# Optimization experiments

Hardware: AMD Instinct MI355X
Metric: run time of the kernel (lower is better)

The kernel has to match this reference:

```python
import jax, jax.numpy as jnp
import numpy as np

B, L, DIM, HEAD_DIM, COND = 16, 1025, 1024, 64, 256
N_HEADS = DIM // HEAD_DIM
EPS = 1e-6


def _make_cos_sin():
    # freqs: head_dim//8 log-spaced frequencies in [pi, 10*pi]
    freqs = np.exp(np.linspace(np.log(np.pi), np.log(10 * np.pi), HEAD_DIM // 8)).astype(np.float32)
    # axial positions on a 32x32 grid (cell centers in [-1, 1]), with a zero pos prepended
    g = np.linspace(-1.0, 1.0, 33, dtype=np.float32)
    g = (g[:-1] + g[1:]) / 2
    hh, ww = np.meshgrid(g, g, indexing='ij')
    pos = np.stack([hh.ravel(), ww.ravel()], axis=-1)          # [1024, 2]
    pos = np.concatenate([np.zeros((1, 2), np.float32), pos])  # [1025, 2]
    theta = np.concatenate([pos[:, 0:1] * freqs, pos[:, 1:2] * freqs], axis=-1)  # [L, head_dim//4]
    return jnp.asarray(np.cos(theta)), jnp.asarray(np.sin(theta))


def setup_inputs() -> dict:
    key = jax.random.key(0)
    kx, kc, kn, kq, ko = jax.random.split(key, 5)
    cos, sin = _make_cos_sin()
    return {
        'x': jax.random.normal(kx, (B, L, DIM), jnp.float32),
        'cond': jax.random.normal(kc, (B, COND), jnp.float32),
        'w_norm': jax.random.normal(kn, (DIM, COND), jnp.float32) * 0.02,   # AdaRMSNorm linear (zero-init in training; random here)
        'w_qkv': jax.random.normal(kq, (3 * DIM, DIM), jnp.float32) * 0.02,
        'w_out': jax.random.normal(ko, (DIM, DIM), jnp.float32) * 0.02,
        'cos': cos,  # [L, head_dim//4]
        'sin': sin,
    }


def _rope(t, cos, sin):
    # partial non-interleaved rotary: rotate first 2*cos.shape[-1] dims, leave the rest
    half = cos.shape[-1]                      # head_dim//4
    t1 = t[..., :half]
    t2 = t[..., half:2 * half]
    rest = t[..., 2 * half:]
    c = cos[None, :, None, :]                 # [1, L, 1, half]
    s = sin[None, :, None, :]
    return jnp.concatenate([t1 * c - t2 * s, t2 * c + t1 * s, rest], axis=-1)


def reference(x, cond, w_norm, w_qkv, w_out, cos, sin):
    skip = x
    # AdaRMSNorm: scale = cond-linear + 1, normalized by rms(x) in fp32
    scale = cond @ w_norm.T + 1.0                                    # [B, D]
    mean_sq = jnp.mean(jnp.square(x.astype(jnp.float32)), axis=-1, keepdims=True)
    xn = x * (scale[:, None, :] * jax.lax.rsqrt(mean_sq + EPS)).astype(x.dtype)
    # QKV projection
    qkv = (xn @ w_qkv.T).reshape(B, L, 3, N_HEADS, HEAD_DIM)
    q, k, v = qkv[:, :, 0], qkv[:, :, 1], qkv[:, :, 2]               # [B, L, H, hd]
    q = _rope(q, cos, sin)
    k = _rope(k, cos, sin)
    # causal attention (flash_attn default softmax scale = head_dim**-0.5)
    sm_scale = 1.0 / jnp.sqrt(jnp.asarray(HEAD_DIM, jnp.float32))
    scores = jnp.einsum('blhd,bmhd->bhlm', q, k) * sm_scale
    causal = jnp.tril(jnp.ones((L, L), bool))
    scores = jnp.where(causal[None, None], scores, jnp.finfo(scores.dtype).min)
    attn = jax.nn.softmax(scores, axis=-1)
    o = jnp.einsum('bhlm,bmhd->blhd', attn, v).reshape(B, L, DIM)
    return o @ w_out.T + skip
```

## Files before the change

kernel.cpp:

```cpp
#include <hip/hip_runtime.h>
#include <hip/hip_bf16.h>
#include <cstdint>

typedef __bf16 bf16;
typedef bf16 bf16x4 __attribute__((ext_vector_type(4)));
typedef bf16 bf16x8 __attribute__((ext_vector_type(8)));
typedef float f32x4 __attribute__((ext_vector_type(4)));
typedef float f32x16 __attribute__((ext_vector_type(16)));
typedef uint32_t u32x4 __attribute__((ext_vector_type(4)));

#define NB 16
#define NL 1025
#define NDIM 1024
#define NHEADS 16
#define NCOND 256
#define NBH (NB*NHEADS)
#define NML (NB*NL)
#define LP 1056
#define NSLOT 17
#define QSCALE (0.125f * 1.44269504088896340736f)

__device__ __forceinline__ void gload16(const void* g, void* l) {
  __builtin_amdgcn_global_load_lds(
      (const __attribute__((address_space(1))) void*)(uintptr_t)g,
      (__attribute__((address_space(3))) void*)(uintptr_t)l,
      16, 0, 0);
}

__device__ __forceinline__ float fexp2(float x) {
  return __builtin_amdgcn_exp2f(x);
}

__device__ __forceinline__ uint32_t cvtpk(float lo, float hi) {
  uint32_t r;
  asm("v_cvt_pk_bf16_f32 %0, %1, %2" : "=v"(r) : "v"(lo), "v"(hi));
  return r;
}

__device__ __forceinline__ f32x16 zero16() {
  f32x16 z;
#pragma unroll
  for (int i = 0; i < 16; ++i) z[i] = 0.f;
  return z;
}

__global__ __launch_bounds__(256) void k_scale(const float* __restrict__ cond,
                                               const float* __restrict__ wn,
                                               float* __restrict__ scl) {
  __shared__ float cs[NCOND];
  const int b = blockIdx.x, t = threadIdx.x;
  cs[t] = cond[b * NCOND + t];
  __syncthreads();
#pragma unroll
  for (int dd = 0; dd < 4; ++dd) {
    const int d = t * 4 + dd;
    const float4* w = (const float4*)(wn + (size_t)d * NCOND);
    float acc = 1.0f;
    for (int c4 = 0; c4 < NCOND / 4; ++c4) {
      float4 wv = w[c4];
      acc += wv.x * cs[c4*4] + wv.y * cs[c4*4+1] + wv.z * cs[c4*4+2] + wv.w * cs[c4*4+3];
    }
    scl[b * NDIM + d] = acc;
  }
}

__global__ __launch_bounds__(256) void k_cast(const float* __restrict__ src,
                                              bf16* __restrict__ dst, int n) {
  const int i = (blockIdx.x * 256 + threadIdx.x) * 4;
  if (i < n) {
    float4 v = *(const float4*)(src + i);
    bf16x4 o;
    o[0] = (bf16)v.x; o[1] = (bf16)v.y; o[2] = (bf16)v.z; o[3] = (bf16)v.w;
    *(bf16x4*)(dst + i) = o;
  }
}

__global__ __launch_bounds__(256) void k_rmsnorm(const float* __restrict__ x,
                                                 const float* __restrict__ scl,
                                                 bf16* __restrict__ xn) {
  const int row = blockIdx.x, t = threadIdx.x;
  const int b = row / NL;
  const float* xr = x + (size_t)row * NDIM;
  float4 v = *(const float4*)(xr + t * 4);
  float ss = v.x*v.x + v.y*v.y + v.z*v.z + v.w*v.w;
#pragma unroll
  for (int o = 1; o < 64; o <<= 1) ss += __shfl_xor(ss, o);
  __shared__ float red[4];
  if ((t & 63) == 0) red[t >> 6] = ss;
  __syncthreads();
  const float tot = red[0] + red[1] + red[2] + red[3];
  const float rn = rsqrtf(tot * (1.0f / NDIM) + 1e-6f);
  const float4 sc = *(const float4*)(scl + b * NDIM + t * 4);
  bf16x4 o4;
  o4[0] = (bf16)(v.x * sc.x * rn);
  o4[1] = (bf16)(v.y * sc.y * rn);
  o4[2] = (bf16)(v.z * sc.z * rn);
  o4[3] = (bf16)(v.w * sc.w * rn);
  *(bf16x4*)(xn + (size_t)row * NDIM + t * 4) = o4;
}

template <int EPI>
__global__ __launch_bounds__(256) void k_gemm(const bf16* __restrict__ A,
                                              const bf16* __restrict__ Bm,
                                              int M, int N, int K,
                                              float* __restrict__ Cf,
                                              const float* __restrict__ skip,
                                              bf16* __restrict__ qro,
                                              bf16* __restrict__ kro,
                                              bf16* __restrict__ vto,
                                              const float* __restrict__ cosT,
                                              const float* __restrict__ sinT) {
  __shared__ bf16 Als[2][128 * 64];
  __shared__ bf16 Bls[2][128 * 64];
  const int t = threadIdx.x;
  const int wave = t >> 6, lane = t & 63;
  const int g = lane >> 4, c = lane & 15;
  const int wm = wave >> 1, wn_ = wave & 1;

  const int nxb = N >> 7;
  const int nwg = gridDim.x;
  const int cpx = nwg >> 3;
  const int bid = blockIdx.x;
  const int swz = (nwg & 7) ? bid : (bid & 7) * cpx + (bid >> 3);
  const int m0 = (swz / nxb) * 128, n0 = (swz % nxb) * 128;
  const int NT = K >> 6;

  const int srow = lane >> 3;
  const int scol = ((lane & 7) ^ srow) * 8;

  f32x4 acc[4][4];
#pragma unroll
  for (int i = 0; i < 4; ++i)
#pragma unroll
    for (int j = 0; j < 4; ++j) acc[i][j] = f32x4{0.f, 0.f, 0.f, 0.f};

  auto stage = [&](int kt, int q) {
    const int k0 = kt << 6;
#pragma unroll
    for (int i = 0; i < 4; ++i) {
      const int seg = wave * 4 + i;
      int arow = m0 + seg * 8 + srow;
      if (arow >= M) arow = M - 1;
      gload16(A + (size_t)arow * K + k0 + scol, &Als[q][seg * 512]);
      const int brow = n0 + seg * 8 + srow;
      gload16(Bm + (size_t)brow * K + k0 + scol, &Bls[q][seg * 512]);
    }
  };

  stage(0, 0);
  for (int kt = 0; kt < NT; ++kt) {
    const int cur = kt & 1;
    if (kt + 1 < NT) {
      stage(kt + 1, cur ^ 1);
      asm volatile("s_waitcnt vmcnt(8)" ::: "memory");
    } else {
      asm volatile("s_waitcnt vmcnt(0)" ::: "memory");
    }
    __builtin_amdgcn_s_barrier();
    asm volatile("" ::: "memory");
#pragma unroll
    for (int kc = 0; kc < 2; ++kc) {
      bf16x8 af[4], bfr[4];
#pragma unroll
      for (int mi = 0; mi < 4; ++mi) {
        const int r = wm * 64 + mi * 16 + c;
        const int gg = ((kc * 4 + g) ^ (c & 7)) * 8;
        af[mi] = *(const bf16x8*)&Als[cur][r * 64 + gg];
      }
#pragma unroll
      for (int ni = 0; ni < 4; ++ni) {
        const int r = wn_ * 64 + ni * 16 + c;
        const int gg = ((kc * 4 + g) ^ (c & 7)) * 8;
        bfr[ni] = *(const bf16x8*)&Bls[cur][r * 64 + gg];
      }
      __builtin_amdgcn_s_setprio(1);
#pragma unroll
      for (int mi = 0; mi < 4; ++mi)
#pragma unroll
        for (int ni = 0; ni < 4; ++ni)
          acc[mi][ni] = __builtin_amdgcn_mfma_f32_16x16x32_bf16(af[mi], bfr[ni], acc[mi][ni], 0, 0, 0);
      __builtin_amdgcn_s_setprio(0);
    }
    asm volatile("" ::: "memory");
    __builtin_amdgcn_s_barrier();
  }

  if (EPI == 1) {
#pragma unroll
    for (int mi = 0; mi < 4; ++mi) {
      const int rb = m0 + wm * 64 + mi * 16 + g * 4;
#pragma unroll
      for (int ni = 0; ni < 4; ++ni) {
        const int col = n0 + wn_ * 64 + ni * 16 + c;
#pragma unroll
        for (int j = 0; j < 4; ++j) {
          const int row = rb + j;
          if (row < M) {
            const size_t idx = (size_t)row * N + col;
            Cf[idx] = acc[mi][ni][j] + skip[idx];
          }
        }
      }
    }
  } else {
    const int ncol0 = n0 + wn_ * 64;
    const int type = ncol0 >> 10;
    const int hd = (ncol0 & 1023) >> 6;
    if (type == 2) {
#pragma unroll
      for (int mi = 0; mi < 4; ++mi) {
        const int rb = m0 + wm * 64 + mi * 16 + g * 4;
        const int b0 = rb / NL, b3 = (rb + 3) / NL;
        if (rb + 3 < M && b0 == b3) {
          const int l0_ = rb - b0 * NL;
          const size_t bhb = (size_t)(b0 * NHEADS + hd) * 64;
#pragma unroll
          for (int ni = 0; ni < 4; ++ni) {
            const int d = ni * 16 + c;
            bf16x4 v4;
#pragma unroll
            for (int j = 0; j < 4; ++j) v4[j] = (bf16)acc[mi][ni][j];
            *(bf16x4*)(vto + (bhb + d) * LP + l0_) = v4;
          }
        } else {
#pragma unroll
          for (int j = 0; j < 4; ++j) {
            const int row = rb + j;
            if (row < M) {
              const int b_ = row / NL, l = row - b_ * NL;
              const size_t bhb = (size_t)(b_ * NHEADS + hd) * 64;
#pragma unroll
              for (int ni = 0; ni < 4; ++ni)
                vto[(bhb + ni * 16 + c) * LP + l] = (bf16)acc[mi][ni][j];
            }
          }
        }
      }
    } else {
      bf16* dst = (type == 0) ? qro : kro;
      const float qs = (type == 0) ? QSCALE : 1.0f;
#pragma unroll
      for (int mi = 0; mi < 4; ++mi) {
        const int rb = m0 + wm * 64 + mi * 16 + g * 4;
#pragma unroll
        for (int j = 0; j < 4; ++j) {
          const int row = rb + j;
          if (row < M) {
            const int b_ = row / NL, l = row - b_ * NL;
            const float cf = cosT[l * 16 + c], sf = sinT[l * 16 + c];
            const float a0 = acc[mi][0][j], a1 = acc[mi][1][j];
            const float r0 = (a0 * cf - a1 * sf) * qs;
            const float r1 = (a1 * cf + a0 * sf) * qs;
            const float r2 = acc[mi][2][j] * qs;
            const float r3 = acc[mi][3][j] * qs;
            const size_t bse = ((size_t)(b_ * NHEADS + hd) * NL + l) * 64;
            dst[bse + c]      = (bf16)r0;
            dst[bse + 16 + c] = (bf16)r1;
            dst[bse + 32 + c] = (bf16)r2;
            dst[bse + 48 + c] = (bf16)r3;
          }
        }
      }
    }
  }
}

__global__ __launch_bounds__(64) void k_attn(const bf16* __restrict__ qr,
                                             const bf16* __restrict__ kr,
                                             const bf16* __restrict__ vt,
                                             bf16* __restrict__ oa) {
  const int bid = blockIdx.x;
  const int lbid = (bid & 7) * (NBH * NSLOT / 8) + (bid >> 3);
  const int slot = lbid % NSLOT, bh = lbid / NSLOT;
  const int b = bh >> 4, h = bh & 15;
  const int lane = threadIdx.x;
  const int ql = lane & 31;
  const int hh = lane >> 5;
  const bf16* qb = qr + (size_t)bh * NL * 64;
  const bf16* kb = kr + (size_t)bh * NL * 64;
  const bf16* vb = vt + (size_t)bh * 64 * LP;

  const int tA = (slot < 16) ? slot : -1;
  const int tB = (slot < 16) ? 31 - slot : 32;
  const bool hasA = (tA >= 0);

  const int q0A = tA * 32, q0B = tB * 32;
  const int qabsA = q0A + ql, qabsB = q0B + ql;

  bf16x8 bQA[4], bQB[4];
  {
    const int qrB = (q0B + ql < NL) ? q0B + ql : NL - 1;
#pragma unroll
    for (int kc = 0; kc < 4; ++kc)
      bQB[kc] = *(const bf16x8*)(qb + (size_t)qrB * 64 + kc * 16 + hh * 8);
    const int qrA = hasA ? q0A + ql : 0;
#pragma unroll
    for (int kc = 0; kc < 4; ++kc)
      bQA[kc] = *(const bf16x8*)(qb + (size_t)qrA * 64 + kc * 16 + hh * 8);
  }

  f32x16 odA0 = zero16(), odA1 = zero16(), odB0 = zero16(), odB1 = zero16();
  float lsA = 0.f, lsB = 0.f;

  const int ntA = hasA ? ((q0A + 31) / 64 + 1) : 0;
  const int qmaxB = (q0B + 31 < NL - 1) ? q0B + 31 : NL - 1;
  const int ntB = qmaxB / 64 + 1;

  bf16x8 aK[2][4];
  auto loadK = [&](int kv0) {
#pragma unroll
    for (int blk = 0; blk < 2; ++blk) {
      int r = kv0 + blk * 32 + ql; if (r >= NL) r = NL - 1;
      const bf16* kp = kb + (size_t)r * 64 + hh * 8;
#pragma unroll
      for (int kc = 0; kc < 4; ++kc)
        aK[blk][kc] = *(const bf16x8*)(kp + kc * 16);
    }
  };
  loadK(0);

  auto smrepack = [&](const f32x16& s0, const f32x16& s1, int kv0, int q0,
                      int qabs, float& ls, bf16x8 (&pa)[4]) {
    const bool needmask = (kv0 + 63 > q0);
#pragma unroll
    for (int blk = 0; blk < 2; ++blk) {
      const f32x16& s = blk ? s1 : s0;
      float p[16];
#pragma unroll
      for (int r = 0; r < 16; ++r) {
        float v = s[r];
        if (needmask) {
          const int kvabs = kv0 + blk * 32 + (r & 3) + 8 * (r >> 2) + 4 * hh;
          if (kvabs > qabs) v = -1e30f;
        }
        p[r] = fexp2(v);
      }
      ls += (((p[0]+p[1])+(p[2]+p[3])) + ((p[4]+p[5])+(p[6]+p[7])))
          + (((p[8]+p[9])+(p[10]+p[11])) + ((p[12]+p[13])+(p[14]+p[15])));
      uint32_t w[8];
#pragma unroll
      for (int a = 0; a < 8; ++a) w[a] = cvtpk(p[2*a], p[2*a+1]);
      const uint32_t sel0 = hh ? w[0] : w[2];
      const uint32_t sel1 = hh ? w[1] : w[3];
      const uint32_t sel2 = hh ? w[4] : w[6];
      const uint32_t sel3 = hh ? w[5] : w[7];
      const uint32_t ex0 = (uint32_t)__shfl_xor((int)sel0, 32);
      const uint32_t ex1 = (uint32_t)__shfl_xor((int)sel1, 32);
      const uint32_t ex2 = (uint32_t)__shfl_xor((int)sel2, 32);
      const uint32_t ex3 = (uint32_t)__shfl_xor((int)sel3, 32);
      u32x4 w0_, w1_;
      w0_[0] = hh ? ex0 : w[0];
      w0_[1] = hh ? ex1 : w[1];
      w0_[2] = hh ? w[2] : ex0;
      w0_[3] = hh ? w[3] : ex1;
      w1_[0] = hh ? ex2 : w[4];
      w1_[1] = hh ? ex3 : w[5];
      w1_[2] = hh ? w[6] : ex2;
      w1_[3] = hh ? w[7] : ex3;
      pa[2*blk]     = __builtin_bit_cast(bf16x8, w0_);
      pa[2*blk + 1] = __builtin_bit_cast(bf16x8, w1_);
    }
  };

  for (int tk = 0; tk < ntB; ++tk) {
    const int kv0 = tk * 64;
    const bool actA = hasA && (tk < ntA);

    bf16x8 vf[2][4];
#pragma unroll
    for (int dblk = 0; dblk < 2; ++dblk) {
      const bf16* vp = vb + (size_t)(dblk * 32 + ql) * LP;
#pragma unroll
      for (int kc = 0; kc < 4; ++kc) {
        int col = kv0 + kc * 16 + hh * 8;
        if (col > LP - 8) col = LP - 8;
        vf[dblk][kc] = *(const bf16x8*)(vp + col);
      }
    }

    bf16x8 paA[4];
    if (actA) {
      f32x16 s0 = zero16(), s1 = zero16();
#pragma unroll
      for (int kc = 0; kc < 4; ++kc)
        s0 = __builtin_amdgcn_mfma_f32_32x32x16_bf16(aK[0][kc], bQA[kc], s0, 0, 0, 0);
#pragma unroll
      for (int kc = 0; kc < 4; ++kc)
        s1 = __builtin_amdgcn_mfma_f32_32x32x16_bf16(aK[1][kc], bQA[kc], s1, 0, 0, 0);
      smrepack(s0, s1, kv0, q0A, qabsA, lsA, paA);
    }

    f32x16 sB0 = zero16(), sB1 = zero16();
#pragma unroll
    for (int kc = 0; kc < 4; ++kc)
      sB0 = __builtin_amdgcn_mfma_f32_32x32x16_bf16(aK[0][kc], bQB[kc], sB0, 0, 0, 0);
#pragma unroll
    for (int kc = 0; kc < 4; ++kc)
      sB1 = __builtin_amdgcn_mfma_f32_32x32x16_bf16(aK[1][kc], bQB[kc], sB1, 0, 0, 0);

    if (tk + 1 < ntB) loadK(kv0 + 64);

    if (actA) {
#pragma unroll
      for (int kc = 0; kc < 4; ++kc) {
        odA0 = __builtin_amdgcn_mfma_f32_32x32x16_bf16(paA[kc], vf[0][kc], odA0, 0, 0, 0);
        odA1 = __builtin_amdgcn_mfma_f32_32x32x16_bf16(paA[kc], vf[1][kc], odA1, 0, 0, 0);
      }
    }

    bf16x8 paB[4];
    smrepack(sB0, sB1, kv0, q0B, qabsB, lsB, paB);

#pragma unroll
    for (int kc = 0; kc < 4; ++kc) {
      odB0 = __builtin_amdgcn_mfma_f32_32x32x16_bf16(paB[kc], vf[0][kc], odB0, 0, 0, 0);
      odB1 = __builtin_amdgcn_mfma_f32_32x32x16_bf16(paB[kc], vf[1][kc], odB1, 0, 0, 0);
    }
  }

  auto fin = [&](int q0, float ls, const f32x16& od0, const f32x16& od1) {
    const float tot = ls + __shfl_xor(ls, 32);
    const float invOwn = 1.0f / tot;
#pragma unroll
    for (int r = 0; r < 16; ++r) {
      const int qrl = (r & 3) + 8 * (r >> 2) + 4 * hh;
      const float inv = __shfl(invOwn, qrl);
      const int row = q0 + qrl;
      if (row < NL) {
        const size_t ob = (size_t)(b * NL + row) * NDIM + h * 64;
        oa[ob + ql]      = (bf16)(od0[r] * inv);
        oa[ob + 32 + ql] = (bf16)(od1[r] * inv);
      }
    }
  };
  if (hasA) fin(q0A, lsA, odA0, odA1);
  fin(q0B, lsB, odB0, odB1);
}

extern "C" void kernel_launch(void* const* d_in, const int* in_sizes, int n_in,
                              void* d_out, int out_size, void* d_ws, size_t ws_size,
                              hipStream_t stream) {
  const float* x     = (const float*)d_in[0];
  const float* cond  = (const float*)d_in[1];
  const float* wnorm = (const float*)d_in[2];
  const float* wqkv  = (const float*)d_in[3];
  const float* wout  = (const float*)d_in[4];
  const float* cosT  = (const float*)d_in[5];
  const float* sinT  = (const float*)d_in[6];
  float* out = (float*)d_out;
  char* ws = (char*)d_ws;

  float* s_scl = (float*)(ws);
  bf16*  s_wq  = (bf16*)(ws + 65536);
  bf16*  s_wo  = (bf16*)(ws + 6356992);
  bf16*  s_xn  = (bf16*)(ws + 8454144);
  bf16*  s_qr  = (bf16*)(ws + 142802944);
  bf16*  s_kr  = (bf16*)(ws + 176390144);
  bf16*  s_vt  = (bf16*)(ws + 209977344);

  k_scale<<<NB, 256, 0, stream>>>(cond, wnorm, s_scl);
  k_cast<<<3072, 256, 0, stream>>>(wqkv, s_wq, 3 * NDIM * NDIM);
  k_cast<<<1024, 256, 0, stream>>>(wout, s_wo, NDIM * NDIM);
  k_rmsnorm<<<NML, 256, 0, stream>>>(x, s_scl, s_xn);
  k_gemm<2><<<3096, 256, 0, stream>>>(s_xn, s_wq, NML, 3 * NDIM, NDIM,
                                      nullptr, nullptr, s_qr, s_kr, s_vt,
                                      cosT, sinT);
  k_attn<<<NBH * NSLOT, 64, 0, stream>>>(s_qr, s_kr, s_vt, s_xn);
  k_gemm<1><<<1032, 256, 0, stream>>>(s_xn, s_wo, NML, NDIM, NDIM,
                                      out, x, nullptr, nullptr, nullptr,
                                      nullptr, nullptr);
}
```

Measured before the change: 427.9 us.

## Use 256x128 GEMM tiles with 512 threads, triple buffering, and fuse prep kernels

The GEMM kernel moves to 512 threads and 256x128 output tiles, so each B tile is reused across twice as many rows. LDS staging goes from double to triple buffering, with loads issued two k-steps ahead and matching waitcnts. The scale and weight-cast kernels are merged into one launch to cut launch overhead. The larger LDS footprint (about 144KB) limits occupancy to one block per CU, and the tail tile now covers more padded rows.

```diff
diff --git a/kernel.cpp b/kernel.cpp
--- a/kernel.cpp
+++ b/kernel.cpp
@@ -44,34 +44,39 @@
   return z;
 }
 
-__global__ __launch_bounds__(256) void k_scale(const float* __restrict__ cond,
-                                               const float* __restrict__ wn,
-                                               float* __restrict__ scl) {
+__global__ __launch_bounds__(256) void k_prep(const float* __restrict__ wqkv,
+                                              const float* __restrict__ wout,
+                                              const float* __restrict__ cond,
+                                              const float* __restrict__ wn,
+                                              bf16* __restrict__ wq,
+                                              bf16* __restrict__ wo,
+                                              float* __restrict__ scl) {
   __shared__ float cs[NCOND];
-  const int b = blockIdx.x, t = threadIdx.x;
-  cs[t] = cond[b * NCOND + t];
-  __syncthreads();
-#pragma unroll
-  for (int dd = 0; dd < 4; ++dd) {
-    const int d = t * 4 + dd;
-    const float4* w = (const float4*)(wn + (size_t)d * NCOND);
-    float acc = 1.0f;
-    for (int c4 = 0; c4 < NCOND / 4; ++c4) {
-      float4 wv = w[c4];
-      acc += wv.x * cs[c4*4] + wv.y * cs[c4*4+1] + wv.z * cs[c4*4+2] + wv.w * cs[c4*4+3];
-    }
-    scl[b * NDIM + d] = acc;
-  }
-}
-
-__global__ __launch_bounds__(256) void k_cast(const float* __restrict__ src,
-                                              bf16* __restrict__ dst, int n) {
-  const int i = (blockIdx.x * 256 + threadIdx.x) * 4;
-  if (i < n) {
+  const int bid = blockIdx.x, t = threadIdx.x;
+  if (bid < 4096) {
+    const float* src = (bid < 3072) ? wqkv : wout;
+    bf16* dst = (bid < 3072) ? wq : wo;
+    const int lb = (bid < 3072) ? bid : bid - 3072;
+    const int i = (lb * 256 + t) * 4;
     float4 v = *(const float4*)(src + i);
     bf16x4 o;
     o[0] = (bf16)v.x; o[1] = (bf16)v.y; o[2] = (bf16)v.z; o[3] = (bf16)v.w;
     *(bf16x4*)(dst + i) = o;
+  } else {
+    const int b = bid - 4096;
+    cs[t] = cond[b * NCOND + t];
+    __syncthreads();
+#pragma unroll
+    for (int dd = 0; dd < 4; ++dd) {
+      const int d = t * 4 + dd;
+      const float4* w = (const float4*)(wn + (size_t)d * NCOND);
+      float acc = 1.0f;
+      for (int c4 = 0; c4 < NCOND / 4; ++c4) {
+        float4 wv = w[c4];
+        acc += wv.x * cs[c4*4] + wv.y * cs[c4*4+1] + wv.z * cs[c4*4+2] + wv.w * cs[c4*4+3];
+      }
+      scl[b * NDIM + d] = acc;
+    }
   }
 }
 
@@ -100,7 +105,7 @@
 }
 
 template <int EPI>
-__global__ __launch_bounds__(256) void k_gemm(const bf16* __restrict__ A,
+__global__ __launch_bounds__(512) void k_gemm(const bf16* __restrict__ A,
                                               const bf16* __restrict__ Bm,
                                               int M, int N, int K,
                                               float* __restrict__ Cf,
@@ -110,8 +115,8 @@
                                               bf16* __restrict__ vto,
                                               const float* __restrict__ cosT,
                                               const float* __restrict__ sinT) {
-  __shared__ bf16 Als[2][128 * 64];
-  __shared__ bf16 Bls[2][128 * 64];
+  __shared__ bf16 Als[3][256 * 64];
+  __shared__ bf16 Bls[3][128 * 64];
   const int t = threadIdx.x;
   const int wave = t >> 6, lane = t & 63;
   const int g = lane >> 4, c = lane & 15;
@@ -122,7 +127,7 @@
   const int cpx = nwg >> 3;
   const int bid = blockIdx.x;
   const int swz = (nwg & 7) ? bid : (bid & 7) * cpx + (bid >> 3);
-  const int m0 = (swz / nxb) * 128, n0 = (swz % nxb) * 128;
+  const int m0 = (swz / nxb) * 256, n0 = (swz % nxb) * 128;
   const int NT = K >> 6;
 
   const int srow = lane >> 3;
@@ -142,17 +147,25 @@
       int arow = m0 + seg * 8 + srow;
       if (arow >= M) arow = M - 1;
       gload16(A + (size_t)arow * K + k0 + scol, &Als[q][seg * 512]);
+    }
+#pragma unroll
+    for (int i = 0; i < 2; ++i) {
+      const int seg = wave * 2 + i;
       const int brow = n0 + seg * 8 + srow;
       gload16(Bm + (size_t)brow * K + k0 + scol, &Bls[q][seg * 512]);
     }
   };
 
   stage(0, 0);
+  stage(1, 1);
+  int q = 0;
   for (int kt = 0; kt < NT; ++kt) {
-    const int cur = kt & 1;
-    if (kt + 1 < NT) {
-      stage(kt + 1, cur ^ 1);
-      asm volatile("s_waitcnt vmcnt(8)" ::: "memory");
+    if (kt + 2 < NT) {
+      int wq = q + 2; if (wq >= 3) wq -= 3;
+      stage(kt + 2, wq);
+      asm volatile("s_waitcnt vmcnt(12)" ::: "memory");
+    } else if (kt + 1 < NT) {
+      asm volatile("s_waitcnt vmcnt(6)" ::: "memory");
     } else {
       asm volatile("s_waitcnt vmcnt(0)" ::: "memory");
     }
@@ -162,42 +175,43 @@
     for (int kc = 0; kc < 2; ++kc) {
       bf16x8 af[4], bfr[4];
 #pragma unroll
-      for (int mi = 0; mi < 4; ++mi) {
-        const int r = wm * 64 + mi * 16 + c;
+      for (int rf = 0; rf < 4; ++rf) {
+        const int r = wm * 64 + rf * 16 + c;
         const int gg = ((kc * 4 + g) ^ (c & 7)) * 8;
-        af[mi] = *(const bf16x8*)&Als[cur][r * 64 + gg];
-      }
-#pragma unroll
-      for (int ni = 0; ni < 4; ++ni) {
-        const int r = wn_ * 64 + ni * 16 + c;
+        af[rf] = *(const bf16x8*)&Als[q][r * 64 + gg];
+      }
+#pragma unroll
+      for (int cf = 0; cf < 4; ++cf) {
+        const int r = wn_ * 64 + cf * 16 + c;
         const int gg = ((kc * 4 + g) ^ (c & 7)) * 8;
-        bfr[ni] = *(const bf16x8*)&Bls[cur][r * 64 + gg];
+        bfr[cf] = *(const bf16x8*)&Bls[q][r * 64 + gg];
       }
       __builtin_amdgcn_s_setprio(1);
 #pragma unroll
-      for (int mi = 0; mi < 4; ++mi)
-#pragma unroll
-        for (int ni = 0; ni < 4; ++ni)
-          acc[mi][ni] = __builtin_amdgcn_mfma_f32_16x16x32_bf16(af[mi], bfr[ni], acc[mi][ni], 0, 0, 0);
+      for (int rf = 0; rf < 4; ++rf)
+#pragma unroll
+        for (int cf = 0; cf < 4; ++cf)
+          acc[rf][cf] = __builtin_amdgcn_mfma_f32_16x16x32_bf16(af[rf], bfr[cf], acc[rf][cf], 0, 0, 0);
       __builtin_amdgcn_s_setprio(0);
     }
     asm volatile("" ::: "memory");
     __builtin_amdgcn_s_barrier();
+    ++q; if (q == 3) q = 0;
   }
 
   if (EPI == 1) {
 #pragma unroll
-    for (int mi = 0; mi < 4; ++mi) {
-      const int rb = m0 + wm * 64 + mi * 16 + g * 4;
-#pragma unroll
-      for (int ni = 0; ni < 4; ++ni) {
-        const int col = n0 + wn_ * 64 + ni * 16 + c;
+    for (int rf = 0; rf < 4; ++rf) {
+      const int rb = m0 + wm * 64 + rf * 16 + g * 4;
+#pragma unroll
+      for (int cf = 0; cf < 4; ++cf) {
+        const int col = n0 + wn_ * 64 + cf * 16 + c;
 #pragma unroll
         for (int j = 0; j < 4; ++j) {
           const int row = rb + j;
           if (row < M) {
             const size_t idx = (size_t)row * N + col;
-            Cf[idx] = acc[mi][ni][j] + skip[idx];
+            Cf[idx] = acc[rf][cf][j] + skip[idx];
           }
         }
       }
@@ -208,18 +222,18 @@
     const int hd = (ncol0 & 1023) >> 6;
     if (type == 2) {
 #pragma unroll
-      for (int mi = 0; mi < 4; ++mi) {
-        const int rb = m0 + wm * 64 + mi * 16 + g * 4;
+      for (int rf = 0; rf < 4; ++rf) {
+        const int rb = m0 + wm * 64 + rf * 16 + g * 4;
         const int b0 = rb / NL, b3 = (rb + 3) / NL;
         if (rb + 3 < M && b0 == b3) {
           const int l0_ = rb - b0 * NL;
           const size_t bhb = (size_t)(b0 * NHEADS + hd) * 64;
 #pragma unroll
-          for (int ni = 0; ni < 4; ++ni) {
-            const int d = ni * 16 + c;
+          for (int cf = 0; cf < 4; ++cf) {
+            const int d = cf * 16 + c;
             bf16x4 v4;
 #pragma unroll
-            for (int j = 0; j < 4; ++j) v4[j] = (bf16)acc[mi][ni][j];
+            for (int j = 0; j < 4; ++j) v4[j] = (bf16)acc[rf][cf][j];
             *(bf16x4*)(vto + (bhb + d) * LP + l0_) = v4;
           }
         } else {
@@ -230,8 +244,8 @@
               const int b_ = row / NL, l = row - b_ * NL;
               const size_t bhb = (size_t)(b_ * NHEADS + hd) * 64;
 #pragma unroll
-              for (int ni = 0; ni < 4; ++ni)
-                vto[(bhb + ni * 16 + c) * LP + l] = (bf16)acc[mi][ni][j];
+              for (int cf = 0; cf < 4; ++cf)
+                vto[(bhb + cf * 16 + c) * LP + l] = (bf16)acc[rf][cf][j];
             }
           }
         }
@@ -240,19 +254,19 @@
       bf16* dst = (type == 0) ? qro : kro;
       const float qs = (type == 0) ? QSCALE : 1.0f;
 #pragma unroll
-      for (int mi = 0; mi < 4; ++mi) {
-        const int rb = m0 + wm * 64 + mi * 16 + g * 4;
+      for (int rf = 0; rf < 4; ++rf) {
+        const int rb = m0 + wm * 64 + rf * 16 + g * 4;
 #pragma unroll
         for (int j = 0; j < 4; ++j) {
           const int row = rb + j;
           if (row < M) {
             const int b_ = row / NL, l = row - b_ * NL;
-            const float cf = cosT[l * 16 + c], sf = sinT[l * 16 + c];
-            const float a0 = acc[mi][0][j], a1 = acc[mi][1][j];
-            const float r0 = (a0 * cf - a1 * sf) * qs;
-            const float r1 = (a1 * cf + a0 * sf) * qs;
-            const float r2 = acc[mi][2][j] * qs;
-            const float r3 = acc[mi][3][j] * qs;
+            const float cf_ = cosT[l * 16 + c], sf = sinT[l * 16 + c];
+            const float a0 = acc[rf][0][j], a1 = acc[rf][1][j];
+            const float r0 = (a0 * cf_ - a1 * sf) * qs;
+            const float r1 = (a1 * cf_ + a0 * sf) * qs;
+            const float r2 = acc[rf][2][j] * qs;
+            const float r3 = acc[rf][3][j] * qs;
             const size_t bse = ((size_t)(b_ * NHEADS + hd) * NL + l) * 64;
             dst[bse + c]      = (bf16)r0;
             dst[bse + 16 + c] = (bf16)r1;
@@ -458,15 +472,13 @@
   bf16*  s_kr  = (bf16*)(ws + 176390144);
   bf16*  s_vt  = (bf16*)(ws + 209977344);
 
-  k_scale<<<NB, 256, 0, stream>>>(cond, wnorm, s_scl);
-  k_cast<<<3072, 256, 0, stream>>>(wqkv, s_wq, 3 * NDIM * NDIM);
-  k_cast<<<1024, 256, 0, stream>>>(wout, s_wo, NDIM * NDIM);
+  k_prep<<<4112, 256, 0, stream>>>(wqkv, wout, cond, wnorm, s_wq, s_wo, s_scl);
   k_rmsnorm<<<NML, 256, 0, stream>>>(x, s_scl, s_xn);
-  k_gemm<2><<<3096, 256, 0, stream>>>(s_xn, s_wq, NML, 3 * NDIM, NDIM,
+  k_gemm<2><<<1560, 512, 0, stream>>>(s_xn, s_wq, NML, 3 * NDIM, NDIM,
                                       nullptr, nullptr, s_qr, s_kr, s_vt,
                                       cosT, sinT);
   k_attn<<<NBH * NSLOT, 64, 0, stream>>>(s_qr, s_kr, s_vt, s_xn);
-  k_gemm<1><<<1032, 256, 0, stream>>>(s_xn, s_wo, NML, NDIM, NDIM,
-                                      out, x, nullptr, nullptr, nullptr,
-                                      nullptr, nullptr);
-}
+  k_gemm<1><<<520, 512, 0, stream>>>(s_xn, s_wo, NML, NDIM, NDIM,
+                                     out, x, nullptr, nullptr, nullptr,
+                                     nullptr, nullptr);
+}
```

Result: slower. 446.9 us (+4.5%).
